# Optimization experiments

Hardware: AMD Instinct MI355X
Metric: run time of the kernel (lower is better)

## Reference

```python
import jax, jax.numpy as jnp
import numpy as np
from jax import lax

B, C, H, W = 32, 1, 224, 224
OUT, K, STRIDE, PAD = 64, 5, 1, 2
D = C * K * K

def _make_weight(key):
    # torch kaiming_uniform_(a=0, fan_in=D, gain=sqrt(2)): bound = sqrt(6/fan_in)
    bound = np.sqrt(6.0 / D)
    w = jax.random.uniform(key, (OUT, D), jnp.float32, -bound, bound)
    w = w.at[0].set(-1.0)
    w = w.at[1].set(1.0)
    return w

def setup_inputs() -> dict:
    key = jax.random.key(0)
    kx, kw = jax.random.split(key)
    x = jax.random.normal(kx, (B, C, H, W), jnp.float32)
    weight = _make_weight(kw)
    return {"x": x, "weight": weight}

def reference(x, weight):
    # im2col: [B, C*K*K, H', W']  (channel-major patch ordering matches torch unfold for C=1)
    patches = lax.conv_general_dilated_patches(
        x, (K, K), (STRIDE, STRIDE), [(PAD, PAD), (PAD, PAD)])
    b, d, hp, wp = patches.shape
    win = patches.reshape(b, d, hp * wp).transpose(0, 2, 1)  # [B, L, D]
    x2 = jnp.sum(win * win, axis=-1, keepdims=True)          # [B, L, 1]
    w2 = jnp.sum(weight * weight, axis=-1)                   # [O]
    xw = jnp.einsum('bld,od->blo', win, weight)              # [B, L, O]
    d2 = jnp.maximum(x2 + w2[None, None, :] - 2.0 * xw, 0.0)
    dist = jnp.sqrt(d2)                                      # [B, L, O]
    return dist.transpose(0, 2, 1).reshape(b, OUT, hp, wp)
```

## Files before the change

### kernel.cpp

```cpp
#include <hip/hip_runtime.h>

#define BB    32
#define HH    224
#define WW    224
#define OUTC  64
#define KK    5
#define PADP  2
#define LL    (HH * WW)
#define GPB   (LL / 4)

__global__ __launch_bounds__(256) void gray_conv_kernel(
    const float* __restrict__ x,
    const float* __restrict__ wgt,
    float* __restrict__ out)
{
    __shared__ float sw2[OUTC];

    const int tid = threadIdx.x;

    if (tid < OUTC) {
        float s = 0.f;
        #pragma unroll
        for (int d = 0; d < 25; ++d) {
            const float v = wgt[tid * 25 + d];
            s = fmaf(v, v, s);
        }
        sw2[tid] = s;
    }
    __syncthreads();

    const int g   = blockIdx.x * 256 + tid;
    const int b   = g / GPB;
    const int gr  = g - b * GPB;
    const int rem = gr * 4;
    const int h   = rem / WW;
    const int w0  = rem - h * WW;

    const float* xb = x + (size_t)b * LL;

    int  xc[8];
    bool okc[8];
    #pragma unroll
    for (int c = 0; c < 8; ++c) {
        const int xx = w0 + c - PADP;
        xc[c]  = min(max(xx, 0), WW - 1);
        okc[c] = (unsigned)xx < (unsigned)WW;
    }

    float p[5][8];
    #pragma unroll
    for (int r = 0; r < KK; ++r) {
        const int  yy  = h + r - PADP;
        const int  yc  = min(max(yy, 0), HH - 1);
        const bool okr = (unsigned)yy < (unsigned)HH;
        const float* xrow = xb + yc * WW;
        #pragma unroll
        for (int c = 0; c < 8; ++c) {
            float v = xrow[xc[c]];
            p[r][c] = (okr && okc[c]) ? v : 0.f;
        }
    }

    float colsq[8];
    #pragma unroll
    for (int c = 0; c < 8; ++c) {
        float s = 0.f;
        #pragma unroll
        for (int r = 0; r < KK; ++r) s = fmaf(p[r][c], p[r][c], s);
        colsq[c] = s;
    }
    float x2[4];
    #pragma unroll
    for (int j = 0; j < 4; ++j) {
        x2[j] = ((colsq[j] + colsq[j + 1]) + (colsq[j + 2] + colsq[j + 3]))
                + colsq[j + 4];
    }

    float* ob = out + (size_t)b * OUTC * LL + rem;

    #pragma unroll 2
    for (int o = 0; o < OUTC; ++o) {
        const float* wrow = wgt + o * 25;
        float wv[25];
        #pragma unroll
        for (int d = 0; d < 25; ++d) wv[d] = wrow[d];
        const float w2 = sw2[o];

        float dot[4];
        #pragma unroll
        for (int j = 0; j < 4; ++j) {
            float s = 0.f;
            #pragma unroll
            for (int r = 0; r < KK; ++r)
                #pragma unroll
                for (int k = 0; k < KK; ++k)
                    s = fmaf(p[r][j + k], wv[r * KK + k], s);
            dot[j] = s;
        }

        float r4[4];
        #pragma unroll
        for (int j = 0; j < 4; ++j) {
            float d2 = fmaf(-2.f, dot[j], x2[j] + w2);
            d2 = fmaxf(d2, 0.f);
            r4[j] = __builtin_amdgcn_sqrtf(d2);
        }
        *reinterpret_cast<float4*>(ob + (size_t)o * LL) =
            make_float4(r4[0], r4[1], r4[2], r4[3]);
    }
}

extern "C" void kernel_launch(void* const* d_in, const int* in_sizes, int n_in,
                              void* d_out, int out_size, void* d_ws, size_t ws_size,
                              hipStream_t stream) {
    const float* x   = (const float*)d_in[0];
    const float* wgt = (const float*)d_in[1];
    float* out       = (float*)d_out;

    const int groups = BB * GPB;
    const int blocks = groups / 256;
    gray_conv_kernel<<<dim3(blocks), dim3(256), 0, stream>>>(x, wgt, out);
}
```

Before: 443.8 us.

## Stage input halo rows in LDS and use nontemporal output stores

Each block cooperatively loads a 10x228 zero-padded input tile into shared memory, and each thread reads its 5x8 patch from there instead of doing clamped, predicated global loads. The dot-product loop is reordered so each weight is loaded once and reused across the four outputs. Output float4 stores become nontemporal to avoid polluting cache with the large write stream. The cost is an extra LDS tile and a barrier per block. The kernel is dominated by the output write, so the gains may be small.

```diff
diff --git a/kernel.cpp b/kernel.cpp
--- a/kernel.cpp
+++ b/kernel.cpp
@@ -9,14 +9,39 @@
 #define LL    (HH * WW)
 #define GPB   (LL / 4)
 
+#define SROWS 10
+#define SCOLS 228
+
+typedef float f4 __attribute__((ext_vector_type(4)));
+
 __global__ __launch_bounds__(256) void gray_conv_kernel(
     const float* __restrict__ x,
     const float* __restrict__ wgt,
     float* __restrict__ out)
 {
+    __shared__ float sx[SROWS * SCOLS];
     __shared__ float sw2[OUTC];
 
     const int tid = threadIdx.x;
+
+    const int g0   = blockIdx.x * 256;
+    const int b    = g0 / GPB;
+    const int gr0  = g0 - b * GPB;
+    const int rem0 = gr0 * 4;
+    const int h0   = rem0 / WW;
+
+    const float* xb = x + (size_t)b * LL;
+
+    for (int i = tid; i < SROWS * SCOLS; i += 256) {
+        const int r    = i / SCOLS;
+        const int c    = i - r * SCOLS;
+        const int grow = h0 - PADP + r;
+        const int gcol = c - PADP;
+        float v = 0.f;
+        if ((unsigned)grow < (unsigned)HH && (unsigned)gcol < (unsigned)WW)
+            v = xb[grow * WW + gcol];
+        sx[i] = v;
+    }
 
     if (tid < OUTC) {
         float s = 0.f;
@@ -29,37 +54,20 @@
     }
     __syncthreads();
 
-    const int g   = blockIdx.x * 256 + tid;
-    const int b   = g / GPB;
+    const int g   = g0 + tid;
     const int gr  = g - b * GPB;
     const int rem = gr * 4;
     const int h   = rem / WW;
     const int w0  = rem - h * WW;
+    const int hl  = h - h0;
 
-    const float* xb = x + (size_t)b * LL;
-
-    int  xc[8];
-    bool okc[8];
-    #pragma unroll
-    for (int c = 0; c < 8; ++c) {
-        const int xx = w0 + c - PADP;
-        xc[c]  = min(max(xx, 0), WW - 1);
-        okc[c] = (unsigned)xx < (unsigned)WW;
-    }
-
+    const float* ps = sx + hl * SCOLS + w0;
     float p[5][8];
     #pragma unroll
-    for (int r = 0; r < KK; ++r) {
-        const int  yy  = h + r - PADP;
-        const int  yc  = min(max(yy, 0), HH - 1);
-        const bool okr = (unsigned)yy < (unsigned)HH;
-        const float* xrow = xb + yc * WW;
+    for (int r = 0; r < KK; ++r)
         #pragma unroll
-        for (int c = 0; c < 8; ++c) {
-            float v = xrow[xc[c]];
-            p[r][c] = (okr && okc[c]) ? v : 0.f;
-        }
-    }
+        for (int c = 0; c < 8; ++c)
+            p[r][c] = ps[r * SCOLS + c];
 
     float colsq[8];
     #pragma unroll
@@ -81,32 +89,27 @@
     #pragma unroll 2
     for (int o = 0; o < OUTC; ++o) {
         const float* wrow = wgt + o * 25;
-        float wv[25];
+        const float  w2   = sw2[o];
+
+        float dot[4] = {0.f, 0.f, 0.f, 0.f};
         #pragma unroll
-        for (int d = 0; d < 25; ++d) wv[d] = wrow[d];
-        const float w2 = sw2[o];
+        for (int r = 0; r < KK; ++r)
+            #pragma unroll
+            for (int k = 0; k < KK; ++k) {
+                const float wv = wrow[r * KK + k];
+                #pragma unroll
+                for (int j = 0; j < 4; ++j)
+                    dot[j] = fmaf(p[r][j + k], wv, dot[j]);
+            }
 
-        float dot[4];
-        #pragma unroll
-        for (int j = 0; j < 4; ++j) {
-            float s = 0.f;
-            #pragma unroll
-            for (int r = 0; r < KK; ++r)
-                #pragma unroll
-                for (int k = 0; k < KK; ++k)
-                    s = fmaf(p[r][j + k], wv[r * KK + k], s);
-            dot[j] = s;
-        }
-
-        float r4[4];
+        f4 r4;
         #pragma unroll
         for (int j = 0; j < 4; ++j) {
             float d2 = fmaf(-2.f, dot[j], x2[j] + w2);
             d2 = fmaxf(d2, 0.f);
             r4[j] = __builtin_amdgcn_sqrtf(d2);
         }
-        *reinterpret_cast<float4*>(ob + (size_t)o * LL) =
-            make_float4(r4[0], r4[1], r4[2], r4[3]);
+        __builtin_nontemporal_store(r4, (f4*)(ob + (size_t)o * LL));
     }
 }
 
```

Result: faster. 429.1 us (-3.3%).
